# Kernel tuning notes

Hardware: AMD Instinct MI355X
Metric: run time of the kernel (lower is better)

Reference implementation:

```python
import jax, jax.numpy as jnp
import numpy as np

NEG = jnp.float32(-1e9)  # -inf surrogate, safe for logsumexp
EPS = 1e-7               # keras.backend.epsilon()


def _ctc_loss(y_true, y_pred):
    """Faithful K.ctc_batch_cost with full input/label lengths.

    y_true: [B, L] int labels in [0, C-2] (blank = C-1, TF convention)
    y_pred: [B, T, C] softmax probabilities
    returns: [B, 1] negative log-likelihood per sample
    """
    B, T, C = y_pred.shape
    L = y_true.shape[1]
    blank = C - 1
    S = 2 * L + 1  # extended label: blank-interleaved

    logp = jnp.log(y_pred + EPS)  # [B, T, C]

    # Extended label sequence [blank, l1, blank, l2, ..., lL, blank]
    ext = jnp.full((B, S), blank, dtype=jnp.int32).at[:, 1::2].set(
        y_true.astype(jnp.int32))  # [B, S]

    # Skip transition (s-2 -> s) allowed iff ext[s] != blank and ext[s] != ext[s-2]
    skip = jnp.concatenate(
        [jnp.zeros((B, 2), dtype=bool),
         (ext[:, 2:] != blank) & (ext[:, 2:] != ext[:, :-2])],
        axis=1)  # [B, S]

    # Gather lattice log-probs once: [B, T, S]
    lp = jnp.take_along_axis(logp, ext[:, None, :], axis=2)

    # alpha at t=0: only states 0 (blank) and 1 (first label) reachable
    alpha0 = jnp.full((B, S), NEG).at[:, 0].set(lp[:, 0, 0]).at[:, 1].set(lp[:, 0, 1])

    def step(alpha, lp_t):
        a1 = alpha                                                     # stay
        a2 = jnp.pad(alpha[:, :-1], ((0, 0), (1, 0)), constant_values=NEG)  # advance 1
        a3 = jnp.pad(alpha[:, :-2], ((0, 0), (2, 0)), constant_values=NEG)  # advance 2
        a3 = jnp.where(skip, a3, NEG)
        new = lp_t + jax.nn.logsumexp(jnp.stack([a1, a2, a3]), axis=0)
        return new, None

    lp_rest = jnp.transpose(lp[:, 1:, :], (1, 0, 2))  # [T-1, B, S]
    alphaT, _ = jax.lax.scan(step, alpha0, lp_rest)

    # Total log-prob ends in last blank or last label
    ll = jax.nn.logsumexp(alphaT[:, S - 2:S], axis=1)  # [B]
    return -ll[:, None]  # [B, 1], matches ctc_batch_cost's expand_dims


def setup_inputs() -> dict:
    key = jax.random.key(0)
    k1, k2 = jax.random.split(key)
    B, T, C, L = 512, 512, 128, 64
    logits = jax.random.normal(k1, (B, T, C), dtype=jnp.float32)
    y_pred = jax.nn.softmax(logits, axis=-1)  # ctc_batch_cost expects probs
    y_true = jax.random.randint(k2, (B, L), 0, C - 1)  # labels exclude blank C-1
    return {"y_true": y_true, "y_pred": y_pred}


def reference(y_true, y_pred):
    return _ctc_loss(y_true, y_pred)
```

## Files before the change

### kernel.cpp

```cpp
#include <hip/hip_runtime.h>


constexpr float EPSF = 1e-7f;
constexpr float LN2F = 0.6931471805599453f;

template<int CTRL>
__device__ __forceinline__ float dpp_mov(float x) {
    return __int_as_float(__builtin_amdgcn_update_dpp(
        0, __float_as_int(x), CTRL, 0xF, 0xF, true));
}

__global__ __launch_bounds__(64)
void ctc_fwd(const int* __restrict__ y_true,
             const float* __restrict__ y_pred,
             float* __restrict__ out)
{
    const int b    = blockIdx.x;
    const int lane = threadIdx.x;

    const char* __restrict__ base =
        (const char*)(y_pred + (size_t)b * 512 * 128);

    const int   lab   = y_true[b * 64 + lane];
    const int   labp  = __shfl_up(lab, 1, 64);
    const float skipf = (lane > 0 && lab != labp) ? 1.0f : 0.0f;
    const bool  l0    = (lane == 0);

    const int offL = lab * 4;
    const int offB = 127 * 4;

    float pLab[32], pBlank[32];

    #pragma unroll
    for (int r = 0; r < 32; ++r) {
        pLab[r]   = *(const float*)(base + r * 512 + offL);
        pBlank[r] = *(const float*)(base + r * 512 + offB);
    }

    float aZ, aA, aB;
    {
        float pb0 = pBlank[0] + EPSF;
        float pl0 = pLab[0]   + EPSF;
        aZ = pb0;
        aA = l0 ? pl0 : 0.0f;
        aB = 0.0f;
    }

    int   shift = 0;
    float red   = 0.0f;

    auto slot = [&](int t, int u, bool doLoad) {
        float pl = pLab[u]   + EPSF;
        float pb = pBlank[u] + EPSF;
        float upA = dpp_mov<0x138>(aA);
        float upB = dpp_mov<0x138>(aB);
        upB = l0 ? aZ : upB;
        float ts = aA + upB;
        ts = fmaf(skipf, upA, ts);
        float nA = pl * ts;
        float nB = pb * (aB + aA);
        aZ *= pb;
        aA = nA; aB = nB;

        if ((u & 7) == 3) {
            float r = fmaxf(fmaxf(aA, aB), aZ);
            r = fmaxf(r, dpp_mov<0x111>(r));
            r = fmaxf(r, dpp_mov<0x112>(r));
            r = fmaxf(r, dpp_mov<0x114>(r));
            r = fmaxf(r, dpp_mov<0x118>(r));
            r = fmaxf(r, dpp_mov<0x142>(r));
            r = fmaxf(r, dpp_mov<0x143>(r));
            red = r;
        }
        if ((u & 7) == 7) {
            int mb = __builtin_amdgcn_readlane(__float_as_int(red), 63);
            int e  = (mb >> 23) & 0xff;
            int f  = 314 - e;
            f = f < 1 ? 1 : (f > 254 ? 254 : f);
            float scale = __int_as_float(f << 23);
            shift += f - 127;
            aA *= scale; aB *= scale; aZ *= scale;
        }
        if (doLoad) {
            int rn = t + 32; rn = rn > 511 ? 511 : rn;
            pLab[u]   = *(const float*)(base + rn * 512 + offL);
            pBlank[u] = *(const float*)(base + rn * 512 + offB);
        }
    };

    for (int blk = 0; blk < 15; ++blk) {
        int t0 = 1 + blk * 32;
        #pragma unroll
        for (int i = 0; i < 32; ++i)
            slot(t0 + i, (1 + i) & 31, true);
    }
    #pragma unroll
    for (int i = 0; i < 31; ++i)
        slot(481 + i, (482 + i - 1) & 31, false);

    float s   = aA + aB;
    float ll2 = __builtin_amdgcn_logf(s);
    if (lane == 63) out[b] = ((float)shift - ll2) * LN2F;
}

extern "C" void kernel_launch(void* const* d_in, const int* in_sizes, int n_in,
                              void* d_out, int out_size, void* d_ws, size_t ws_size,
                              hipStream_t stream)
{
    const int*   y_true = (const int*)d_in[0];
    const float* y_pred = (const float*)d_in[1];
    float*       out    = (float*)d_out;

    const int B = out_size;
    ctc_fwd<<<dim3(B), dim3(64), 0, stream>>>(y_true, y_pred, out);
}
```

Baseline: 191.7 us.

## Stage probability rows through LDS with coalesced float4 loads and pipelined buffers

```diff
diff --git a/kernel.cpp b/kernel.cpp
--- a/kernel.cpp
+++ b/kernel.cpp
@@ -18,51 +18,54 @@
     const int b    = blockIdx.x;
     const int lane = threadIdx.x;
 
-    const char* __restrict__ base =
-        (const char*)(y_pred + (size_t)b * 512 * 128);
+    const float4* __restrict__ gsrc =
+        (const float4*)(y_pred + (size_t)b * 512 * 128);
+
+    __shared__ __align__(16) float lds[2 * 2048];
 
     const int   lab   = y_true[b * 64 + lane];
     const int   labp  = __shfl_up(lab, 1, 64);
     const float skipf = (lane > 0 && lab != labp) ? 1.0f : 0.0f;
     const bool  l0    = (lane == 0);
 
-    const int offL = lab * 4;
-    const int offB = 127 * 4;
+    float4 regs[3][8];
 
-    float pLab[32], pBlank[32];
+    auto issueLoads = [&](int chunk, int set) {
+        #pragma unroll
+        for (int k = 0; k < 8; ++k)
+            regs[set][k] = gsrc[chunk * 512 + k * 64 + lane];
+    };
+    auto writeChunk = [&](int chunk, int set) {
+        float* dst = &lds[(chunk & 1) * 2048];
+        #pragma unroll
+        for (int k = 0; k < 8; ++k)
+            *(float4*)(dst + k * 256 + lane * 4) = regs[set][k];
+    };
 
-    #pragma unroll
-    for (int r = 0; r < 32; ++r) {
-        pLab[r]   = *(const float*)(base + r * 512 + offL);
-        pBlank[r] = *(const float*)(base + r * 512 + offB);
-    }
+    float plr[4], pbr[4];
+    auto issueRead = [&](int t) {
+        int tn = t > 511 ? 511 : t;
+        const float* rb = &lds[((tn >> 4) & 1) * 2048 + (tn & 15) * 128];
+        plr[t & 3] = rb[lab];
+        pbr[t & 3] = rb[127];
+    };
 
     float aZ, aA, aB;
-    {
-        float pb0 = pBlank[0] + EPSF;
-        float pl0 = pLab[0]   + EPSF;
-        aZ = pb0;
-        aA = l0 ? pl0 : 0.0f;
-        aB = 0.0f;
-    }
-
     int   shift = 0;
     float red   = 0.0f;
 
-    auto slot = [&](int t, int u, bool doLoad) {
-        float pl = pLab[u]   + EPSF;
-        float pb = pBlank[u] + EPSF;
+    auto consume = [&](int t, int j) {
+        float pl = plr[j & 3] + EPSF;
+        float pb = pbr[j & 3] + EPSF;
         float upA = dpp_mov<0x138>(aA);
         float upB = dpp_mov<0x138>(aB);
         upB = l0 ? aZ : upB;
-        float ts = aA + upB;
-        ts = fmaf(skipf, upA, ts);
+        float ts = fmaf(skipf, upA, aA + upB);
         float nA = pl * ts;
         float nB = pb * (aB + aA);
         aZ *= pb;
         aA = nA; aB = nB;
-
-        if ((u & 7) == 3) {
+        if ((j & 7) == 3) {
             float r = fmaxf(fmaxf(aA, aB), aZ);
             r = fmaxf(r, dpp_mov<0x111>(r));
             r = fmaxf(r, dpp_mov<0x112>(r));
@@ -72,7 +75,7 @@
             r = fmaxf(r, dpp_mov<0x143>(r));
             red = r;
         }
-        if ((u & 7) == 7) {
+        if ((j & 7) == 7) {
             int mb = __builtin_amdgcn_readlane(__float_as_int(red), 63);
             int e  = (mb >> 23) & 0xff;
             int f  = 314 - e;
@@ -81,22 +84,52 @@
             shift += f - 127;
             aA *= scale; aB *= scale; aZ *= scale;
         }
-        if (doLoad) {
-            int rn = t + 32; rn = rn > 511 ? 511 : rn;
-            pLab[u]   = *(const float*)(base + rn * 512 + offL);
-            pBlank[u] = *(const float*)(base + rn * 512 + offB);
-        }
+        issueRead(t + 4);
     };
 
-    for (int blk = 0; blk < 15; ++blk) {
-        int t0 = 1 + blk * 32;
-        #pragma unroll
-        for (int i = 0; i < 32; ++i)
-            slot(t0 + i, (1 + i) & 31, true);
+    issueLoads(0, 0); issueLoads(1, 1); issueLoads(2, 2);
+    writeChunk(0, 0);
+    issueRead(0); issueRead(1); issueRead(2); issueRead(3);
+    {
+        float pb0 = pbr[0] + EPSF;
+        float pl0 = plr[0] + EPSF;
+        aZ = pb0;
+        aA = l0 ? pl0 : 0.0f;
+        aB = 0.0f;
     }
+    issueRead(4);
+
+    issueLoads(3, 0);
+    writeChunk(1, 1);
     #pragma unroll
-    for (int i = 0; i < 31; ++i)
-        slot(481 + i, (482 + i - 1) & 31, false);
+    for (int j = 1; j < 16; ++j) consume(j, j);
+
+    for (int cb = 1; cb <= 28; cb += 3) {
+        {
+            int c = cb;
+            if (c + 3 < 32) issueLoads(c + 3, 1);
+            writeChunk(c + 1, 2);
+            #pragma unroll
+            for (int j = 0; j < 16; ++j) consume(16 * c + j, j);
+        }
+        {
+            int c = cb + 1;
+            if (c + 3 < 32) issueLoads(c + 3, 2);
+            writeChunk(c + 1, 0);
+            #pragma unroll
+            for (int j = 0; j < 16; ++j) consume(16 * c + j, j);
+        }
+        {
+            int c = cb + 2;
+            if (c + 3 < 32) issueLoads(c + 3, 0);
+            writeChunk(c + 1, 1);
+            #pragma unroll
+            for (int j = 0; j < 16; ++j) consume(16 * c + j, j);
+        }
+    }
+
+    #pragma unroll
+    for (int j = 0; j < 16; ++j) consume(16 * 31 + j, j);
 
     float s   = aA + aB;
     float ll2 = __builtin_amdgcn_logf(s);
```

Result: slower. 216.8 us (+13.1%).
